# Kernel optimization log

Hardware: AMD Instinct MI355X
Metric: run time of the kernel (lower is better)

The kernel has to match this reference:

```python
import jax, jax.numpy as jnp
import numpy as np

COORD_DIM = 2
NUM_CHANNELS = 3
LATENT = 128
HIDDEN = 64
N0 = 8192
RADIUS = 0.035
RADII = (RADIUS, 2.0 * RADIUS)
ITER_COUNT = 3


def _radius_edges(y, x, r):
    # y: (Ny,d) source points, x: (Nx,d) query points -> edge lists (src into y, dst into x)
    d2 = ((x[:, None, :] - y[None, :, :]) ** 2).sum(-1)
    dst, src = np.nonzero(d2 <= r * r)
    return jnp.asarray(src, jnp.int32), jnp.asarray(dst, jnp.int32)


def setup_inputs():
    rng = np.random.default_rng(0)
    coords_np = rng.uniform(size=(COORD_DIM, N0)).astype(np.float32)
    c0 = coords_np.T            # (N0, d) fine level
    c1 = coords_np[:, ::2].T    # (N1, d) coarse level (stride-2 subsample)
    r_cross = max(RADII)
    e01_src, e01_dst = _radius_edges(c0, c1, r_cross)   # GK_0_1: y=lvl0, x=lvl1
    e10_src, e10_dst = _radius_edges(c1, c0, r_cross)   # GK_1_0: y=lvl1, x=lvl0
    e00_src, e00_dst = _radius_edges(c0, c0, RADII[0])  # GK_0_0
    e11_src, e11_dst = _radius_edges(c1, c1, RADII[1])  # GK_1_1

    key = jax.random.key(0)
    ks = iter(jax.random.split(key, 40))

    def lin(fi, fo):
        return jax.random.normal(next(ks), (fi, fo), jnp.float32) / np.float32(np.sqrt(fi))

    inp = dict(
        coords=jnp.asarray(coords_np),
        samples=jax.random.normal(next(ks), (N0, NUM_CHANNELS), jnp.float32),
        sigma=jax.random.uniform(next(ks), (1,), jnp.float32),
        fc_lift_w=lin(NUM_CHANNELS, LATENT), fc_lift_b=jnp.zeros((LATENT,), jnp.float32),
        fc_proj_w=lin(LATENT, NUM_CHANNELS), fc_proj_b=jnp.zeros((NUM_CHANNELS,), jnp.float32),
        W0_w=lin(LATENT, LATENT), W0_b=jnp.zeros((LATENT,), jnp.float32),
        W1_w=lin(LATENT, LATENT), W1_b=jnp.zeros((LATENT,), jnp.float32),
    )
    for name in ("gk00", "gk01", "gk10", "gk11"):
        inp[name + "_w1"] = lin(2 * COORD_DIM, HIDDEN)
        inp[name + "_b1"] = jnp.zeros((HIDDEN,), jnp.float32)
        inp[name + "_w2"] = lin(HIDDEN, LATENT)
        inp[name + "_b2"] = jnp.zeros((LATENT,), jnp.float32)
    inp.update(e00_src=e00_src, e00_dst=e00_dst, e01_src=e01_src, e01_dst=e01_dst,
               e10_src=e10_src, e10_dst=e10_dst, e11_src=e11_src, e11_dst=e11_dst)
    return inp


def _gno(xc, yc, f_y, src, dst, w1, b1, w2, b2, num_x):
    # gather -> edge kernel MLP on concat coords -> modulate by f_y -> scatter-mean
    e = jnp.concatenate([yc[src], xc[dst]], axis=1)        # (E, 2d)
    k = jax.nn.gelu(e @ w1 + b1) @ w2 + b2                 # (E, C) kernel values
    msg = k * f_y[src]                                     # 'linear' integral transform
    out = jax.ops.segment_sum(msg, dst, num_segments=num_x)
    cnt = jax.ops.segment_sum(jnp.ones(src.shape, msg.dtype), dst, num_segments=num_x)
    return out / jnp.maximum(cnt, 1.0)[:, None]


def reference(coords, samples, sigma,
              fc_lift_w, fc_lift_b, fc_proj_w, fc_proj_b,
              W0_w, W0_b, W1_w, W1_b,
              gk00_w1, gk00_b1, gk00_w2, gk00_b2,
              gk01_w1, gk01_b1, gk01_w2, gk01_b2,
              gk10_w1, gk10_b1, gk10_w2, gk10_b2,
              gk11_w1, gk11_b1, gk11_w2, gk11_b2,
              e00_src, e00_dst, e01_src, e01_dst,
              e10_src, e10_dst, e11_src, e11_dst):
    c0 = coords.T            # (N0, d)
    c1 = coords[:, ::2].T    # (N1, d)
    n0, n1 = c0.shape[0], c1.shape[0]
    v_down0 = samples @ fc_lift_w + fc_lift_b   # lifted features, never overwritten at level 0
    v_up0 = v_down0
    v_up1 = None
    for _ in range(ITER_COUNT):
        # downward pass (l = 1)
        vd = _gno(c1, c0, v_down0, e01_src, e01_dst, gk01_w1, gk01_b1, gk01_w2, gk01_b2, n1)
        if v_up1 is not None:
            vd = vd + v_up1
        v_down1 = jax.nn.relu(vd)
        # bottom level update
        v_up1 = jax.nn.relu(v_down1 @ W1_w + W1_b
                            + _gno(c1, c1, v_down1, e11_src, e11_dst, gk11_w1, gk11_b1, gk11_w2, gk11_b2, n1))
        # upward pass (l = 0)
        vu = _gno(c0, c1, v_up1, e10_src, e10_dst, gk10_w1, gk10_b1, gk10_w2, gk10_b2, n0)
        vu = vu + v_down0 @ W0_w + W0_b \
             + _gno(c0, c0, v_down0, e00_src, e00_dst, gk00_w1, gk00_b1, gk00_w2, gk00_b2, n0)
        v_up0 = jax.nn.relu(vu)
    return v_up0 @ fc_proj_w + fc_proj_b   # (N0, num_channels)
```

## Files before the change

kernel.cpp:

```cpp
#include <hip/hip_runtime.h>
#include <hip/hip_bf16.h>

typedef __attribute__((ext_vector_type(8))) short s8;
typedef __attribute__((ext_vector_type(4))) float f4;

#define TILE 128

__device__ __forceinline__ float gelu_fast(float x) {
    float x2 = x * x;
    float k2 = x * fmaf(x2, 0.10294326f, 2.30220819f);
    float e  = __builtin_amdgcn_exp2f(k2);
    float r  = __builtin_amdgcn_rcpf(e + 1.f);
    return fmaf(-x, r, x);
}

__device__ __forceinline__ unsigned pack_bf16x2(float a, float b) {
    __hip_bfloat162 h = __float22bfloat162_rn(make_float2(a, b));
    return *(unsigned*)&h;
}

__device__ __forceinline__ short f2bf_bits(float v) {
    __hip_bfloat16 b = __float2bfloat16(v);
    return *(short*)&b;
}

struct RP { const int* edst; int E; int N; int* rowptr; };

__global__ void rowptr4_kernel(RP a, RP b, RP c, RP d) {
    RP g = (blockIdx.y == 0) ? a : (blockIdx.y == 1) ? b : (blockIdx.y == 2) ? c : d;
    int i = blockIdx.x * blockDim.x + threadIdx.x;
    if (i >= g.E) return;
    int dd = g.edst[i];
    int p  = (i == 0) ? -1 : g.edst[i - 1];
    for (int r = p + 1; r <= dd; ++r) g.rowptr[r] = i;
    if (i == g.E - 1)
        for (int r = dd + 1; r <= g.N; ++r) g.rowptr[r] = g.E;
}

__global__ __launch_bounds__(128) void pack_w2_kernel(
    const float* __restrict__ wa, const float* __restrict__ wb,
    const float* __restrict__ wc, const float* __restrict__ wd,
    short* __restrict__ out)
{
    const int g = blockIdx.x >> 2, T = blockIdx.x & 3;
    const float* w2 = (g == 0) ? wa : (g == 1) ? wb : (g == 2) ? wc : wd;
    short* dst = out + (size_t)g * 8192;
    const int t = threadIdx.x;
    const int w = t >> 6, lane = t & 63, q = (lane >> 4), n = lane & 15;
#pragma unroll
    for (int s = 0; s < 2; ++s)
#pragma unroll
        for (int j = 0; j < 8; ++j) {
            int k  = s * 32 + q * 8 + j;
            int ch = 64 * w + 4 * n + T;
            dst[((((w * 4 + T) * 2 + s) * 64) + lane) * 8 + j] =
                f2bf_bits(w2[k * 128 + ch]);
        }
}

struct GnoP {
    const float* fy;
    const int* esrc;
    const int* edst;
    const float* w1;
    const float* b1;
    const short* w2;
    const float* b2;
    float* acc;
    int E, sx, sy, pad;
};

__device__ __forceinline__ int seg_end(unsigned long long m0, unsigned long long m1, int a) {
    if (a < 64) {
        unsigned long long r = m0 >> a;
        if (r) return a + (int)__builtin_ctzll(r) + 1;
        return 64 + (int)__builtin_ctzll(m1) + 1;
    }
    unsigned long long r = m1 >> (a - 64);
    return a + (int)__builtin_ctzll(r) + 1;
}

__global__ __launch_bounds__(128) void gno_edge_kernel(
    const float* __restrict__ coords, int n0, GnoP A, GnoP B, int ntA)
{
    const GnoP P = (blockIdx.x < ntA) ? A : B;
    const int tile = (blockIdx.x < ntA) ? blockIdx.x : blockIdx.x - ntA;
    const int t = threadIdx.x;
    const int w = t >> 6, lane = t & 63, q = lane >> 4, n = lane & 15;
    const int e0 = tile * TILE;
    const int te = min(TILE, P.E - e0);

    __shared__ __align__(16) float s_crd[(TILE + 16) * 4];
    __shared__ int s_off[TILE];
    __shared__ int s_dst[TILE];
    __shared__ unsigned long long s_mask[2];
    __shared__ __align__(16) short s_gb[2][16 * 72];

    {
        int e = min(e0 + t, P.E - 1);
        int sv = P.esrc[e];
        int dv = P.edst[e];
        s_off[t] = sv * 128;
        s_dst[t] = dv;
        f4 c4 = {coords[(long)sv * P.sy], coords[n0 + (long)sv * P.sy],
                 coords[(long)dv * P.sx], coords[n0 + (long)dv * P.sx]};
        *(f4*)&s_crd[t * 4] = c4;
        if (t < 16) *(f4*)&s_crd[(TILE + t) * 4] = c4;
    }

    const int h0 = 2 * (lane & 31);
    const float wA0 = P.w1[h0],       wA1 = P.w1[h0 + 1];
    const float wB0 = P.w1[64 + h0],  wB1 = P.w1[65 + h0];
    const float wC0 = P.w1[128 + h0], wC1 = P.w1[129 + h0];
    const float wD0 = P.w1[192 + h0], wD1 = P.w1[193 + h0];
    const float b10 = P.b1[h0],       b11 = P.b1[h0 + 1];

    s8 bfrag[4][2];
    const s8* w2f = (const s8*)P.w2;
#pragma unroll
    for (int T = 0; T < 4; ++T)
#pragma unroll
        for (int s = 0; s < 2; ++s)
            bfrag[T][s] = w2f[((w * 4 + T) * 2 + s) * 64 + lane];
    const f4 b2c = *(const f4*)&P.b2[w * 64 + 4 * n];
    f4 b2i[4];
#pragma unroll
    for (int T = 0; T < 4; ++T) { f4 z = {b2c[T], b2c[T], b2c[T], b2c[T]}; b2i[T] = z; }

    const float* fyl = P.fy + (w * 64 + 4 * n);

    __syncthreads();

    {
        int idx = w * 64 + lane;
        bool fl = (idx < te) && (idx == te - 1 || s_dst[idx + 1] != s_dst[idx]);
        unsigned long long m = __ballot(fl);
        if (lane == 0) s_mask[w] = m;
    }
    __syncthreads();
    const unsigned long long m0 = s_mask[0], m1 = s_mask[1];

    int g0 = 0;
    int b = seg_end(m0, m1, 0);
    f4 fvc[4];
#pragma unroll
    for (int r = 0; r < 4; ++r) {
        int row = q * 4 + r;
        if (row < b) fvc[r] = *(const f4*)&fyl[s_off[row]];
        else { f4 z = {0.f, 0.f, 0.f, 0.f}; fvc[r] = z; }
    }
    f4 accr = {0.f, 0.f, 0.f, 0.f};
    int gbp = 0;
    const int jh = lane >> 5;

    while (true) {
#pragma unroll
        for (int i = 0; i < 4; ++i) {
            int j = 4 * i + 2 * jh + w;
            const f4 crd = *(const f4*)&s_crd[(g0 + j) * 4];
            float x0 = fmaf(crd[0], wA0, fmaf(crd[1], wB0,
                       fmaf(crd[2], wC0, fmaf(crd[3], wD0, b10))));
            float x1 = fmaf(crd[0], wA1, fmaf(crd[1], wB1,
                       fmaf(crd[2], wC1, fmaf(crd[3], wD1, b11))));
            *(unsigned*)&s_gb[gbp][j * 72 + h0] = pack_bf16x2(gelu_fast(x0), gelu_fast(x1));
        }
        __syncthreads();
        const s8 a0 = *(const s8*)&s_gb[gbp][n * 72 + q * 8];
        const s8 a1 = *(const s8*)&s_gb[gbp][n * 72 + q * 8 + 32];
        f4 c[4];
#pragma unroll
        for (int T = 0; T < 4; ++T) {
            f4 z = __builtin_amdgcn_mfma_f32_16x16x32_bf16(a0, bfrag[T][0], b2i[T], 0, 0, 0);
            c[T] = __builtin_amdgcn_mfma_f32_16x16x32_bf16(a1, bfrag[T][1], z, 0, 0, 0);
        }
#pragma unroll
        for (int r = 0; r < 4; ++r)
#pragma unroll
            for (int T = 0; T < 4; ++T)
                accr[T] = fmaf(c[T][r], fvc[r][T], accr[T]);

        int gn = g0 + 16, bn = b;
        const bool endseg = (gn >= b);
        if (endseg) {
            gn = b;
            if (gn < te) bn = seg_end(m0, m1, gn);
            const int dcur = s_dst[g0];
#pragma unroll
            for (int T = 0; T < 4; ++T) {
                float v = accr[T];
                v += __shfl_xor(v, 16, 64);
                v += __shfl_xor(v, 32, 64);
                if (q == 0)
                    atomicAdd(&P.acc[(long)dcur * 128 + w * 64 + 4 * n + T], v);
            }
            f4 z = {0.f, 0.f, 0.f, 0.f};
            accr = z;
        }
        if (gn >= te) break;
#pragma unroll
        for (int r = 0; r < 4; ++r) {
            int row = gn + q * 4 + r;
            if (row < bn) fvc[r] = *(const f4*)&fyl[s_off[row]];
            else { f4 z = {0.f, 0.f, 0.f, 0.f}; fvc[r] = z; }
        }
        g0 = gn; b = bn;
        gbp ^= 1;
    }
}

__global__ void zero_kernel(float* __restrict__ p, long n) {
    long i = ((long)blockIdx.x * 256 + threadIdx.x) * 4;
    if (i < n) { f4 z = {0.f, 0.f, 0.f, 0.f}; *(f4*)&p[i] = z; }
}

__global__ __launch_bounds__(256) void epi0001_kernel(
    float* __restrict__ acc, const int* __restrict__ rp00, int N0,
    const int* __restrict__ rp01, float* __restrict__ vd0zero, long ntot)
{
    long idx = (long)blockIdx.x * 256 + threadIdx.x;
    if (idx >= ntot) return;
    int d = (int)(idx >> 7);
    float deg;
    if (d < N0) { deg = (float)(rp00[d + 1] - rp00[d]); vd0zero[idx] = 0.f; }
    else        { deg = (float)(rp01[d - N0 + 1] - rp01[d - N0]); }
    acc[idx] = acc[idx] / fmaxf(deg, 1.f);
}

__global__ __launch_bounds__(128) void relu_mm_kernel(
    const float* __restrict__ base, float* __restrict__ accu,
    const int* __restrict__ rowptr, float* __restrict__ w1t,
    const float* __restrict__ W, const float* __restrict__ bias,
    float* __restrict__ vout, float* __restrict__ zbuf, int R)
{
    const int r0 = blockIdx.x * 8;
    const int t = threadIdx.x;
    __shared__ float s_x[8 * 128];
#pragma unroll
    for (int j = 0; j < 8; ++j) {
        int r = r0 + j;
        long o = (long)r * 128 + t;
        float v = base[o];
        if (accu) {
            float deg = (float)(rowptr[r + 1] - rowptr[r]);
            float u = fmaxf(accu[o] / fmaxf(deg, 1.f) + w1t[o], 0.f);
            v += u;
            accu[o] = 0.f;
        } else if (zbuf) {
            zbuf[o] = 0.f;
        }
        v = fmaxf(v, 0.f);
        s_x[j * 128 + t] = v;
        vout[o] = v;
    }
    __syncthreads();
    float acc[8];
    const float bc = bias[t];
#pragma unroll
    for (int j = 0; j < 8; ++j) acc[j] = bc;
#pragma unroll 4
    for (int hh = 0; hh < 128; ++hh) {
        float wv = W[hh * 128 + t];
#pragma unroll
        for (int j = 0; j < 8; ++j) acc[j] += s_x[j * 128 + hh] * wv;
    }
#pragma unroll
    for (int j = 0; j < 8; ++j)
        w1t[(long)(r0 + j) * 128 + t] = acc[j];
}

__global__ __launch_bounds__(256) void epi11_kernel(
    float* __restrict__ acc, const int* __restrict__ rowptr,
    const float* __restrict__ w1t, int N)
{
    long idx = (long)blockIdx.x * 256 + threadIdx.x;
    if (idx >= (long)N * 128) return;
    int d = (int)(idx >> 7);
    float deg = (float)(rowptr[d + 1] - rowptr[d]);
    acc[idx] = fmaxf(acc[idx] / fmaxf(deg, 1.f) + w1t[idx], 0.f);
}

__global__ __launch_bounds__(128) void lift_mm_kernel(
    const float* __restrict__ samples, const float* __restrict__ LW,
    const float* __restrict__ Lb, const float* __restrict__ W0,
    const float* __restrict__ W0b, float* __restrict__ vout,
    float* __restrict__ w0t, int R)
{
    const int r0 = blockIdx.x * 8;
    const int t = threadIdx.x;
    __shared__ float s_x[8 * 128];
#pragma unroll
    for (int j = 0; j < 8; ++j) {
        int r = r0 + j;
        float s0 = samples[r * 3 + 0], s1 = samples[r * 3 + 1], s2 = samples[r * 3 + 2];
        float v = s0 * LW[t] + s1 * LW[128 + t] + s2 * LW[256 + t] + Lb[t];
        s_x[j * 128 + t] = v;
        vout[(long)r * 128 + t] = v;
    }
    __syncthreads();
    float acc[8];
    const float bc = W0b[t];
#pragma unroll
    for (int j = 0; j < 8; ++j) acc[j] = bc;
#pragma unroll 4
    for (int hh = 0; hh < 128; ++hh) {
        float wv = W0[hh * 128 + t];
#pragma unroll
        for (int j = 0; j < 8; ++j) acc[j] += s_x[j * 128 + hh] * wv;
    }
#pragma unroll
    for (int j = 0; j < 8; ++j)
        w0t[(long)(r0 + j) * 128 + t] = acc[j];
}

__global__ __launch_bounds__(128) void epi_proj_kernel(
    const float* __restrict__ acc, const int* __restrict__ rowptr,
    const float* __restrict__ add0, const float* __restrict__ add1,
    const float* __restrict__ projw, const float* __restrict__ projb,
    float* __restrict__ fout, int N)
{
    const int d = blockIdx.x, t = threadIdx.x;
    float deg = (float)(rowptr[d + 1] - rowptr[d]);
    long o = (long)d * 128 + t;
    float res = fmaxf(acc[o] / fmaxf(deg, 1.f) + add0[o] + add1[o], 0.f);
    float p0 = res * projw[t * 3 + 0];
    float p1 = res * projw[t * 3 + 1];
    float p2 = res * projw[t * 3 + 2];
#pragma unroll
    for (int off = 32; off > 0; off >>= 1) {
        p0 += __shfl_down(p0, off);
        p1 += __shfl_down(p1, off);
        p2 += __shfl_down(p2, off);
    }
    __shared__ float sred[6];
    if ((t & 63) == 0) { int w = t >> 6; sred[w * 3 + 0] = p0; sred[w * 3 + 1] = p1; sred[w * 3 + 2] = p2; }
    __syncthreads();
    if (t < 3) fout[d * 3 + t] = sred[t] + sred[3 + t] + projb[t];
}

extern "C" void kernel_launch(void* const* d_in, const int* in_sizes, int n_in,
                              void* d_out, int out_size, void* d_ws, size_t ws_size,
                              hipStream_t stream)
{
    const float* coords  = (const float*)d_in[0];
    const float* samples = (const float*)d_in[1];
    const float* lift_w  = (const float*)d_in[3];
    const float* lift_b  = (const float*)d_in[4];
    const float* proj_w  = (const float*)d_in[5];
    const float* proj_b  = (const float*)d_in[6];
    const float* W0_w    = (const float*)d_in[7];
    const float* W0_b    = (const float*)d_in[8];
    const float* W1_w    = (const float*)d_in[9];
    const float* W1_b    = (const float*)d_in[10];
    const float *gw1[4], *gb1[4], *gw2[4], *gb2[4];
    for (int g = 0; g < 4; ++g) {
        gw1[g] = (const float*)d_in[11 + 4 * g + 0];
        gb1[g] = (const float*)d_in[11 + 4 * g + 1];
        gw2[g] = (const float*)d_in[11 + 4 * g + 2];
        gb2[g] = (const float*)d_in[11 + 4 * g + 3];
    }
    const int* es[4]; const int* ed[4]; int E[4];
    for (int g = 0; g < 4; ++g) {
        es[g] = (const int*)d_in[27 + 2 * g];
        ed[g] = (const int*)d_in[27 + 2 * g + 1];
        E[g]  = in_sizes[27 + 2 * g];
    }

    const int N0 = in_sizes[0] / 2;
    const int N1 = (N0 + 1) / 2;

    float* ws = (float*)d_ws;
    float* v_down0 = ws;
    float* w0term  = v_down0 + (size_t)N0 * 128;
    float* gno00o  = w0term  + (size_t)N0 * 128;
    float* gno01b  = gno00o  + (size_t)N0 * 128;
    float* v_down1 = gno01b  + (size_t)N1 * 128;
    float* w1term  = v_down1 + (size_t)N1 * 128;
    float* v_up1   = w1term  + (size_t)N1 * 128;
    short* w2pack  = (short*)(v_up1 + (size_t)N1 * 128);
    int*   rp      = (int*)(w2pack + 4 * 8192);
    int* rp00 = rp;
    int* rp01 = rp00 + (N0 + 1);
    int* rp10 = rp01 + (N1 + 1);
    int* rp11 = rp10 + (N0 + 1);

    {
        int maxE = E[0];
        for (int g = 1; g < 4; ++g) maxE = max(maxE, E[g]);
        RP a = {ed[0], E[0], N0, rp00};
        RP b = {ed[1], E[1], N1, rp01};
        RP c = {ed[2], E[2], N0, rp10};
        RP d = {ed[3], E[3], N1, rp11};
        dim3 grid((maxE + 255) / 256, 4);
        rowptr4_kernel<<<grid, 256, 0, stream>>>(a, b, c, d);
    }
    pack_w2_kernel<<<16, 128, 0, stream>>>(gw2[0], gw2[1], gw2[2], gw2[3], w2pack);

    const long n00 = (long)N0 * 128, n11 = (long)N1 * 128;

    zero_kernel<<<(int)((n00 + n11) / 4 + 255) / 256, 256, 0, stream>>>(gno00o, n00 + n11);
    lift_mm_kernel<<<N0 / 8, 128, 0, stream>>>(samples, lift_w, lift_b, W0_w, W0_b,
                                               v_down0, w0term, N0);

    GnoP P00 = {v_down0, es[0], ed[0], gw1[0], gb1[0], w2pack + 0 * 8192, gb2[0], gno00o, E[0], 1, 1, 0};
    GnoP P01 = {v_down0, es[1], ed[1], gw1[1], gb1[1], w2pack + 1 * 8192, gb2[1], gno01b, E[1], 2, 1, 0};
    GnoP P11 = {v_down1, es[3], ed[3], gw1[3], gb1[3], w2pack + 3 * 8192, gb2[3], v_up1,  E[3], 2, 2, 0};
    GnoP P10 = {v_up1,   es[2], ed[2], gw1[2], gb1[2], w2pack + 2 * 8192, gb2[2], v_down0, E[2], 1, 2, 0};

    {
        int tA = (E[0] + TILE - 1) / TILE, tB = (E[1] + TILE - 1) / TILE;
        gno_edge_kernel<<<tA + tB, 128, 0, stream>>>(coords, N0, P00, P01, tA);
    }
    epi0001_kernel<<<(int)((n00 + n11) + 255) / 256, 256, 0, stream>>>(
        gno00o, rp00, N0, rp01, v_down0, n00 + n11);

    for (int it = 0; it < 3; ++it) {
        relu_mm_kernel<<<N1 / 8, 128, 0, stream>>>(
            gno01b, (it == 0) ? nullptr : v_up1, rp11, w1term, W1_w, W1_b,
            v_down1, (it == 0) ? v_up1 : nullptr, N1);
        int tt = (E[3] + TILE - 1) / TILE;
        gno_edge_kernel<<<tt, 128, 0, stream>>>(coords, N0, P11, P11, tt);
    }
    epi11_kernel<<<(int)(n11 + 255) / 256, 256, 0, stream>>>(v_up1, rp11, w1term, N1);

    {
        int tt = (E[2] + TILE - 1) / TILE;
        gno_edge_kernel<<<tt, 128, 0, stream>>>(coords, N0, P10, P10, tt);
    }
    epi_proj_kernel<<<N0, 128, 0, stream>>>(v_down0, rp10, w0term, gno00o,
                                            proj_w, proj_b, (float*)d_out, N0);
}
```

Baseline: 356.5 us.

## Split edge-kernel MLP over hidden dim per wave to remove block barriers

Each wave now computes half of the hidden units and all 128 output channels in its own shared buffer. This removes the per-iteration __syncthreads and the cross-wave mask exchange. The edge tile shrinks to 64 so one wave ballot covers the tile, and the kernel now requests 3 blocks per SM via launch bounds. Both waves issue atomics with their partial sums, so atomic traffic doubles. bf16 packing switches to a cheaper round-half-up bit trick, and the W2 pack layout changes to match.

```diff
diff --git a/kernel.cpp b/kernel.cpp
--- a/kernel.cpp
+++ b/kernel.cpp
@@ -4,7 +4,7 @@
 typedef __attribute__((ext_vector_type(8))) short s8;
 typedef __attribute__((ext_vector_type(4))) float f4;
 
-#define TILE 128
+#define TILE 64
 
 __device__ __forceinline__ float gelu_fast(float x) {
     float x2 = x * x;
@@ -14,9 +14,10 @@
     return fmaf(-x, r, x);
 }
 
-__device__ __forceinline__ unsigned pack_bf16x2(float a, float b) {
-    __hip_bfloat162 h = __float22bfloat162_rn(make_float2(a, b));
-    return *(unsigned*)&h;
+__device__ __forceinline__ unsigned pack_bf16x2_fast(float a, float b) {
+    unsigned ua = __builtin_bit_cast(unsigned, a) + 0x8000u;
+    unsigned ub = __builtin_bit_cast(unsigned, b) + 0x8000u;
+    return __builtin_amdgcn_perm(ub, ua, 0x07060302u);
 }
 
 __device__ __forceinline__ short f2bf_bits(float v) {
@@ -42,19 +43,18 @@
     const float* __restrict__ wc, const float* __restrict__ wd,
     short* __restrict__ out)
 {
-    const int g = blockIdx.x >> 2, T = blockIdx.x & 3;
+    const int g = blockIdx.x;
     const float* w2 = (g == 0) ? wa : (g == 1) ? wb : (g == 2) ? wc : wd;
     short* dst = out + (size_t)g * 8192;
     const int t = threadIdx.x;
-    const int w = t >> 6, lane = t & 63, q = (lane >> 4), n = lane & 15;
-#pragma unroll
-    for (int s = 0; s < 2; ++s)
+    const int s = t >> 6, lane = t & 63, q = (lane >> 4), n = lane & 15;
+#pragma unroll
+    for (int T = 0; T < 8; ++T)
 #pragma unroll
         for (int j = 0; j < 8; ++j) {
-            int k  = s * 32 + q * 8 + j;
-            int ch = 64 * w + 4 * n + T;
-            dst[((((w * 4 + T) * 2 + s) * 64) + lane) * 8 + j] =
-                f2bf_bits(w2[k * 128 + ch]);
+            int h  = 32 * s + q * 8 + j;
+            int ch = 8 * n + T;
+            dst[((s * 8 + T) * 64 + lane) * 8 + j] = f2bf_bits(w2[h * 128 + ch]);
         }
 }
 
@@ -70,33 +70,26 @@
     int E, sx, sy, pad;
 };
 
-__device__ __forceinline__ int seg_end(unsigned long long m0, unsigned long long m1, int a) {
-    if (a < 64) {
-        unsigned long long r = m0 >> a;
-        if (r) return a + (int)__builtin_ctzll(r) + 1;
-        return 64 + (int)__builtin_ctzll(m1) + 1;
-    }
-    unsigned long long r = m1 >> (a - 64);
-    return a + (int)__builtin_ctzll(r) + 1;
-}
-
-__global__ __launch_bounds__(128) void gno_edge_kernel(
+__device__ __forceinline__ int seg_end1(unsigned long long m, int a) {
+    return a + 1 + (int)__builtin_ctzll(m >> a);
+}
+
+__global__ __launch_bounds__(128, 3) void gno_edge_kernel(
     const float* __restrict__ coords, int n0, GnoP A, GnoP B, int ntA)
 {
     const GnoP P = (blockIdx.x < ntA) ? A : B;
     const int tile = (blockIdx.x < ntA) ? blockIdx.x : blockIdx.x - ntA;
     const int t = threadIdx.x;
-    const int w = t >> 6, lane = t & 63, q = lane >> 4, n = lane & 15;
+    const int wv = t >> 6, lane = t & 63, q = lane >> 4, n = lane & 15;
     const int e0 = tile * TILE;
     const int te = min(TILE, P.E - e0);
 
     __shared__ __align__(16) float s_crd[(TILE + 16) * 4];
     __shared__ int s_off[TILE];
     __shared__ int s_dst[TILE];
-    __shared__ unsigned long long s_mask[2];
-    __shared__ __align__(16) short s_gb[2][16 * 72];
-
-    {
+    __shared__ __align__(16) short s_gb[2][16 * 40];
+
+    if (t < TILE) {
         int e = min(e0 + t, P.E - 1);
         int sv = P.esrc[e];
         int dv = P.edst[e];
@@ -108,103 +101,110 @@
         if (t < 16) *(f4*)&s_crd[(TILE + t) * 4] = c4;
     }
 
-    const int h0 = 2 * (lane & 31);
+    const int hl = 2 * (lane & 15);
+    const int h0 = 32 * wv + hl;
     const float wA0 = P.w1[h0],       wA1 = P.w1[h0 + 1];
     const float wB0 = P.w1[64 + h0],  wB1 = P.w1[65 + h0];
     const float wC0 = P.w1[128 + h0], wC1 = P.w1[129 + h0];
     const float wD0 = P.w1[192 + h0], wD1 = P.w1[193 + h0];
     const float b10 = P.b1[h0],       b11 = P.b1[h0 + 1];
 
-    s8 bfrag[4][2];
+    s8 bfrag[8];
     const s8* w2f = (const s8*)P.w2;
 #pragma unroll
-    for (int T = 0; T < 4; ++T)
-#pragma unroll
-        for (int s = 0; s < 2; ++s)
-            bfrag[T][s] = w2f[((w * 4 + T) * 2 + s) * 64 + lane];
-    const f4 b2c = *(const f4*)&P.b2[w * 64 + 4 * n];
-    f4 b2i[4];
-#pragma unroll
-    for (int T = 0; T < 4; ++T) { f4 z = {b2c[T], b2c[T], b2c[T], b2c[T]}; b2i[T] = z; }
-
-    const float* fyl = P.fy + (w * 64 + 4 * n);
+    for (int T = 0; T < 8; ++T)
+        bfrag[T] = w2f[(wv * 8 + T) * 64 + lane];
+
+    f4 b2a = {0.f, 0.f, 0.f, 0.f}, b2b = {0.f, 0.f, 0.f, 0.f};
+    if (wv == 0) {
+        b2a = *(const f4*)&P.b2[8 * n];
+        b2b = *(const f4*)&P.b2[8 * n + 4];
+    }
+    const float* fyl = P.fy + 8 * n;
+    short* gb = &s_gb[wv][0];
+    const int je = 4 * (lane >> 4);
 
     __syncthreads();
 
-    {
-        int idx = w * 64 + lane;
-        bool fl = (idx < te) && (idx == te - 1 || s_dst[idx + 1] != s_dst[idx]);
-        unsigned long long m = __ballot(fl);
-        if (lane == 0) s_mask[w] = m;
-    }
-    __syncthreads();
-    const unsigned long long m0 = s_mask[0], m1 = s_mask[1];
+    bool fl = (lane < te) && (lane == te - 1 || s_dst[lane + 1] != s_dst[lane]);
+    const unsigned long long m = __ballot(fl);
 
     int g0 = 0;
-    int b = seg_end(m0, m1, 0);
-    f4 fvc[4];
+    int b = seg_end1(m, 0);
+    f4 fva[4], fvb[4];
 #pragma unroll
     for (int r = 0; r < 4; ++r) {
         int row = q * 4 + r;
-        if (row < b) fvc[r] = *(const f4*)&fyl[s_off[row]];
-        else { f4 z = {0.f, 0.f, 0.f, 0.f}; fvc[r] = z; }
-    }
-    f4 accr = {0.f, 0.f, 0.f, 0.f};
-    int gbp = 0;
-    const int jh = lane >> 5;
+        if (row < b) {
+            const float* p = &fyl[s_off[row]];
+            fva[r] = *(const f4*)p;
+            fvb[r] = *(const f4*)(p + 4);
+        } else {
+            f4 z = {0.f, 0.f, 0.f, 0.f};
+            fva[r] = z; fvb[r] = z;
+        }
+    }
+    float accr[8] = {0.f, 0.f, 0.f, 0.f, 0.f, 0.f, 0.f, 0.f};
 
     while (true) {
 #pragma unroll
         for (int i = 0; i < 4; ++i) {
-            int j = 4 * i + 2 * jh + w;
+            int j = je + i;
             const f4 crd = *(const f4*)&s_crd[(g0 + j) * 4];
             float x0 = fmaf(crd[0], wA0, fmaf(crd[1], wB0,
                        fmaf(crd[2], wC0, fmaf(crd[3], wD0, b10))));
             float x1 = fmaf(crd[0], wA1, fmaf(crd[1], wB1,
                        fmaf(crd[2], wC1, fmaf(crd[3], wD1, b11))));
-            *(unsigned*)&s_gb[gbp][j * 72 + h0] = pack_bf16x2(gelu_fast(x0), gelu_fast(x1));
-        }
-        __syncthreads();
-        const s8 a0 = *(const s8*)&s_gb[gbp][n * 72 + q * 8];
-        const s8 a1 = *(const s8*)&s_gb[gbp][n * 72 + q * 8 + 32];
-        f4 c[4];
-#pragma unroll
-        for (int T = 0; T < 4; ++T) {
-            f4 z = __builtin_amdgcn_mfma_f32_16x16x32_bf16(a0, bfrag[T][0], b2i[T], 0, 0, 0);
-            c[T] = __builtin_amdgcn_mfma_f32_16x16x32_bf16(a1, bfrag[T][1], z, 0, 0, 0);
-        }
-#pragma unroll
-        for (int r = 0; r < 4; ++r)
-#pragma unroll
-            for (int T = 0; T < 4; ++T)
-                accr[T] = fmaf(c[T][r], fvc[r][T], accr[T]);
+            *(unsigned*)&gb[j * 40 + hl] = pack_bf16x2_fast(gelu_fast(x0), gelu_fast(x1));
+        }
+        const s8 a = *(const s8*)&gb[n * 40 + q * 8];
+#pragma unroll
+        for (int Tp = 0; Tp < 4; ++Tp) {
+            f4 z = {0.f, 0.f, 0.f, 0.f};
+            f4 c0 = __builtin_amdgcn_mfma_f32_16x16x32_bf16(a, bfrag[2 * Tp], z, 0, 0, 0);
+            f4 c1 = __builtin_amdgcn_mfma_f32_16x16x32_bf16(a, bfrag[2 * Tp + 1], z, 0, 0, 0);
+            const int T0 = 2 * Tp, T1 = 2 * Tp + 1;
+            const float bb0 = (T0 < 4) ? b2a[T0 & 3] : b2b[T0 & 3];
+            const float bb1 = (T1 < 4) ? b2a[T1 & 3] : b2b[T1 & 3];
+#pragma unroll
+            for (int r = 0; r < 4; ++r) {
+                float f0 = (T0 < 4) ? fva[r][T0 & 3] : fvb[r][T0 & 3];
+                float f1 = (T1 < 4) ? fva[r][T1 & 3] : fvb[r][T1 & 3];
+                accr[T0] = fmaf(c0[r] + bb0, f0, accr[T0]);
+                accr[T1] = fmaf(c1[r] + bb1, f1, accr[T1]);
+            }
+        }
 
         int gn = g0 + 16, bn = b;
         const bool endseg = (gn >= b);
         if (endseg) {
             gn = b;
-            if (gn < te) bn = seg_end(m0, m1, gn);
+            if (gn < te) bn = seg_end1(m, gn);
             const int dcur = s_dst[g0];
-#pragma unroll
-            for (int T = 0; T < 4; ++T) {
+            float* ap = &P.acc[(long)dcur * 128 + 8 * n];
+#pragma unroll
+            for (int T = 0; T < 8; ++T) {
                 float v = accr[T];
                 v += __shfl_xor(v, 16, 64);
                 v += __shfl_xor(v, 32, 64);
-                if (q == 0)
-                    atomicAdd(&P.acc[(long)dcur * 128 + w * 64 + 4 * n + T], v);
+                if (q == 0) atomicAdd(&ap[T], v);
+                accr[T] = 0.f;
             }
-            f4 z = {0.f, 0.f, 0.f, 0.f};
-            accr = z;
         }
         if (gn >= te) break;
 #pragma unroll
         for (int r = 0; r < 4; ++r) {
             int row = gn + q * 4 + r;
-            if (row < bn) fvc[r] = *(const f4*)&fyl[s_off[row]];
-            else { f4 z = {0.f, 0.f, 0.f, 0.f}; fvc[r] = z; }
+            if (row < bn) {
+                const float* p = &fyl[s_off[row]];
+                fva[r] = *(const f4*)p;
+                fvb[r] = *(const f4*)(p + 4);
+            } else {
+                f4 z = {0.f, 0.f, 0.f, 0.f};
+                fva[r] = z; fvb[r] = z;
+            }
         }
         g0 = gn; b = bn;
-        gbp ^= 1;
     }
 }
 
@@ -393,7 +393,7 @@
         dim3 grid((maxE + 255) / 256, 4);
         rowptr4_kernel<<<grid, 256, 0, stream>>>(a, b, c, d);
     }
-    pack_w2_kernel<<<16, 128, 0, stream>>>(gw2[0], gw2[1], gw2[2], gw2[3], w2pack);
+    pack_w2_kernel<<<4, 128, 0, stream>>>(gw2[0], gw2[1], gw2[2], gw2[3], w2pack);
 
     const long n00 = (long)N0 * 128, n11 = (long)N1 * 128;
 
```

New measurement: 692.1 us. +94.1%, slower.

## Process 32-edge chunks per iteration and use cheaper bf16 packing

Applied to the files above, without the earlier changes.

The edge loop now handles up to 32 edges per iteration instead of 16. It computes GELU hidden activations for 32 rows, issues a second MFMA pair only when the segment still has more than 16 rows, and gathers two sets of source feature rows up front. This is meant to halve the per-chunk barriers and loop overhead, and to increase memory-level parallelism for the gathers. It also swaps the bf16 round-to-nearest-even conversion for an add-0x8000-and-permute trick, which rounds half away and does not handle NaN. The trade-offs are more registers and LDS per block and wasted GELU work on short segments.

```diff
diff --git a/kernel.cpp b/kernel.cpp
--- a/kernel.cpp
+++ b/kernel.cpp
@@ -14,9 +14,10 @@
     return fmaf(-x, r, x);
 }
 
-__device__ __forceinline__ unsigned pack_bf16x2(float a, float b) {
-    __hip_bfloat162 h = __float22bfloat162_rn(make_float2(a, b));
-    return *(unsigned*)&h;
+__device__ __forceinline__ unsigned pack_bf16x2_fast(float a, float b) {
+    unsigned ua = __builtin_bit_cast(unsigned, a) + 0x8000u;
+    unsigned ub = __builtin_bit_cast(unsigned, b) + 0x8000u;
+    return __builtin_amdgcn_perm(ub, ua, 0x07060302u);
 }
 
 __device__ __forceinline__ short f2bf_bits(float v) {
@@ -90,11 +91,11 @@
     const int e0 = tile * TILE;
     const int te = min(TILE, P.E - e0);
 
-    __shared__ __align__(16) float s_crd[(TILE + 16) * 4];
+    __shared__ __align__(16) float s_crd[(TILE + 32) * 4];
     __shared__ int s_off[TILE];
     __shared__ int s_dst[TILE];
     __shared__ unsigned long long s_mask[2];
-    __shared__ __align__(16) short s_gb[2][16 * 72];
+    __shared__ __align__(16) short s_gb[2][32 * 72];
 
     {
         int e = min(e0 + t, P.E - 1);
@@ -105,7 +106,7 @@
         f4 c4 = {coords[(long)sv * P.sy], coords[n0 + (long)sv * P.sy],
                  coords[(long)dv * P.sx], coords[n0 + (long)dv * P.sx]};
         *(f4*)&s_crd[t * 4] = c4;
-        if (t < 16) *(f4*)&s_crd[(TILE + t) * 4] = c4;
+        if (t < 32) *(f4*)&s_crd[(TILE + t) * 4] = c4;
     }
 
     const int h0 = 2 * (lane & 31);
@@ -142,12 +143,14 @@
 
     int g0 = 0;
     int b = seg_end(m0, m1, 0);
-    f4 fvc[4];
+    f4 fv0[4], fv1[4];
 #pragma unroll
     for (int r = 0; r < 4; ++r) {
-        int row = q * 4 + r;
-        if (row < b) fvc[r] = *(const f4*)&fyl[s_off[row]];
-        else { f4 z = {0.f, 0.f, 0.f, 0.f}; fvc[r] = z; }
+        int row0 = q * 4 + r, row1 = 16 + q * 4 + r;
+        if (row0 < b) fv0[r] = *(const f4*)&fyl[s_off[row0]];
+        else { f4 z = {0.f, 0.f, 0.f, 0.f}; fv0[r] = z; }
+        if (row1 < b) fv1[r] = *(const f4*)&fyl[s_off[row1]];
+        else { f4 z = {0.f, 0.f, 0.f, 0.f}; fv1[r] = z; }
     }
     f4 accr = {0.f, 0.f, 0.f, 0.f};
     int gbp = 0;
@@ -155,31 +158,51 @@
 
     while (true) {
 #pragma unroll
-        for (int i = 0; i < 4; ++i) {
+        for (int i = 0; i < 8; ++i) {
             int j = 4 * i + 2 * jh + w;
             const f4 crd = *(const f4*)&s_crd[(g0 + j) * 4];
             float x0 = fmaf(crd[0], wA0, fmaf(crd[1], wB0,
                        fmaf(crd[2], wC0, fmaf(crd[3], wD0, b10))));
             float x1 = fmaf(crd[0], wA1, fmaf(crd[1], wB1,
                        fmaf(crd[2], wC1, fmaf(crd[3], wD1, b11))));
-            *(unsigned*)&s_gb[gbp][j * 72 + h0] = pack_bf16x2(gelu_fast(x0), gelu_fast(x1));
+            *(unsigned*)&s_gb[gbp][j * 72 + h0] = pack_bf16x2_fast(gelu_fast(x0), gelu_fast(x1));
         }
         __syncthreads();
-        const s8 a0 = *(const s8*)&s_gb[gbp][n * 72 + q * 8];
-        const s8 a1 = *(const s8*)&s_gb[gbp][n * 72 + q * 8 + 32];
-        f4 c[4];
-#pragma unroll
-        for (int T = 0; T < 4; ++T) {
-            f4 z = __builtin_amdgcn_mfma_f32_16x16x32_bf16(a0, bfrag[T][0], b2i[T], 0, 0, 0);
-            c[T] = __builtin_amdgcn_mfma_f32_16x16x32_bf16(a1, bfrag[T][1], z, 0, 0, 0);
-        }
-#pragma unroll
-        for (int r = 0; r < 4; ++r)
-#pragma unroll
-            for (int T = 0; T < 4; ++T)
-                accr[T] = fmaf(c[T][r], fvc[r][T], accr[T]);
-
-        int gn = g0 + 16, bn = b;
+        const short* gb = &s_gb[gbp][0];
+        const int cnt = min(32, b - g0);
+        {
+            const s8 a0 = *(const s8*)&gb[n * 72 + q * 8];
+            const s8 a1 = *(const s8*)&gb[n * 72 + q * 8 + 32];
+            f4 c[4];
+#pragma unroll
+            for (int T = 0; T < 4; ++T) {
+                f4 z = __builtin_amdgcn_mfma_f32_16x16x32_bf16(a0, bfrag[T][0], b2i[T], 0, 0, 0);
+                c[T] = __builtin_amdgcn_mfma_f32_16x16x32_bf16(a1, bfrag[T][1], z, 0, 0, 0);
+            }
+#pragma unroll
+            for (int r = 0; r < 4; ++r)
+#pragma unroll
+                for (int T = 0; T < 4; ++T)
+                    accr[T] = fmaf(c[T][r], fv0[r][T], accr[T]);
+        }
+        if (cnt > 16) {
+            const s8 a0 = *(const s8*)&gb[(16 + n) * 72 + q * 8];
+            const s8 a1 = *(const s8*)&gb[(16 + n) * 72 + q * 8 + 32];
+            f4 c[4];
+#pragma unroll
+            for (int T = 0; T < 4; ++T) {
+                f4 z = {0.f, 0.f, 0.f, 0.f};
+                z = __builtin_amdgcn_mfma_f32_16x16x32_bf16(a0, bfrag[T][0], z, 0, 0, 0);
+                c[T] = __builtin_amdgcn_mfma_f32_16x16x32_bf16(a1, bfrag[T][1], z, 0, 0, 0);
+            }
+#pragma unroll
+            for (int r = 0; r < 4; ++r)
+#pragma unroll
+                for (int T = 0; T < 4; ++T)
+                    accr[T] = fmaf(c[T][r], fv1[r][T], accr[T]);
+        }
+
+        int gn = g0 + cnt, bn = b;
         const bool endseg = (gn >= b);
         if (endseg) {
             gn = b;
@@ -199,9 +222,11 @@
         if (gn >= te) break;
 #pragma unroll
         for (int r = 0; r < 4; ++r) {
-            int row = gn + q * 4 + r;
-            if (row < bn) fvc[r] = *(const f4*)&fyl[s_off[row]];
-            else { f4 z = {0.f, 0.f, 0.f, 0.f}; fvc[r] = z; }
+            int row0 = gn + q * 4 + r, row1 = gn + 16 + q * 4 + r;
+            if (row0 < bn) fv0[r] = *(const f4*)&fyl[s_off[row0]];
+            else { f4 z = {0.f, 0.f, 0.f, 0.f}; fv0[r] = z; }
+            if (row1 < bn) fv1[r] = *(const f4*)&fyl[s_off[row1]];
+            else { f4 z = {0.f, 0.f, 0.f, 0.f}; fv1[r] = z; }
         }
         g0 = gn; b = bn;
         gbp ^= 1;
```

Result: slower. 383.3 us (+7.5%).

## Merge setup kernels into one prep launch and fold degree normalization into consumers

Applied to the files above, without the earlier changes.

Combines the zeroing, weight-packing, rowptr-building and lift/W0 matmul kernels into a single prep kernel that dispatches on block index. It removes the epi0001 pass by applying the degree normalizations in relu_mm and epi_proj, and moves the v_down0 zeroing into epi11. It also replaces the round-to-nearest-even bf16 pack with a bias-add-and-permute that rounds ties away from zero, which changes numerics slightly. The goal is fewer launches and less extra memory traffic, in exchange for a heterogeneous prep grid and a repeated division inside the loop.

```diff
diff --git a/kernel.cpp b/kernel.cpp
--- a/kernel.cpp
+++ b/kernel.cpp
@@ -14,9 +14,10 @@
     return fmaf(-x, r, x);
 }
 
-__device__ __forceinline__ unsigned pack_bf16x2(float a, float b) {
-    __hip_bfloat162 h = __float22bfloat162_rn(make_float2(a, b));
-    return *(unsigned*)&h;
+__device__ __forceinline__ unsigned pack_bf16x2_fast(float a, float b) {
+    unsigned ua = __builtin_bit_cast(unsigned, a) + 0x8000u;
+    unsigned ub = __builtin_bit_cast(unsigned, b) + 0x8000u;
+    return __builtin_amdgcn_perm(ub, ua, 0x07060302u);
 }
 
 __device__ __forceinline__ short f2bf_bits(float v) {
@@ -24,38 +25,85 @@
     return *(short*)&b;
 }
 
-struct RP { const int* edst; int E; int N; int* rowptr; };
-
-__global__ void rowptr4_kernel(RP a, RP b, RP c, RP d) {
-    RP g = (blockIdx.y == 0) ? a : (blockIdx.y == 1) ? b : (blockIdx.y == 2) ? c : d;
-    int i = blockIdx.x * blockDim.x + threadIdx.x;
-    if (i >= g.E) return;
-    int dd = g.edst[i];
-    int p  = (i == 0) ? -1 : g.edst[i - 1];
-    for (int r = p + 1; r <= dd; ++r) g.rowptr[r] = i;
-    if (i == g.E - 1)
-        for (int r = dd + 1; r <= g.N; ++r) g.rowptr[r] = g.E;
-}
-
-__global__ __launch_bounds__(128) void pack_w2_kernel(
-    const float* __restrict__ wa, const float* __restrict__ wb,
-    const float* __restrict__ wc, const float* __restrict__ wd,
-    short* __restrict__ out)
-{
-    const int g = blockIdx.x >> 2, T = blockIdx.x & 3;
-    const float* w2 = (g == 0) ? wa : (g == 1) ? wb : (g == 2) ? wc : wd;
-    short* dst = out + (size_t)g * 8192;
+struct PrepArgs {
+    float* zbase; long zn4;
+    const float* w2s[4]; short* w2pack;
+    const int* edst[4]; int E[4]; int N[4]; int* rowptr[4]; int rbPer;
+    const float *samples, *LW, *Lb, *W0, *W0b;
+    float *vout, *w0t;
+    int zb;
+};
+
+__global__ __launch_bounds__(256) void prep_kernel(PrepArgs A) {
+    __shared__ float s_x[16 * 128];
+    int bid = blockIdx.x;
     const int t = threadIdx.x;
-    const int w = t >> 6, lane = t & 63, q = (lane >> 4), n = lane & 15;
-#pragma unroll
-    for (int s = 0; s < 2; ++s)
+    if (bid < A.zb) {
+        long i = (long)bid * 256 + t;
+        if (i < A.zn4) { f4 z = {0.f, 0.f, 0.f, 0.f}; *(f4*)&A.zbase[i * 4] = z; }
+        return;
+    }
+    bid -= A.zb;
+    if (bid < 16) {
+        if (t < 128) {
+            const int g = bid >> 2, T = bid & 3;
+            const float* w2 = A.w2s[g];
+            short* dst = A.w2pack + (size_t)g * 8192;
+            const int w = t >> 6, lane = t & 63, q = (lane >> 4), n = lane & 15;
+#pragma unroll
+            for (int s = 0; s < 2; ++s)
+#pragma unroll
+                for (int j = 0; j < 8; ++j) {
+                    int k  = s * 32 + q * 8 + j;
+                    int ch = 64 * w + 4 * n + T;
+                    dst[((((w * 4 + T) * 2 + s) * 64) + lane) * 8 + j] =
+                        f2bf_bits(w2[k * 128 + ch]);
+                }
+        }
+        return;
+    }
+    bid -= 16;
+    if (bid < 4 * A.rbPer) {
+        const int g = bid / A.rbPer;
+        const int i = (bid % A.rbPer) * 256 + t;
+        const int* ed = A.edst[g]; const int E = A.E[g]; const int N = A.N[g];
+        int* rp = A.rowptr[g];
+        if (i < E) {
+            int dd = ed[i];
+            int p  = (i == 0) ? -1 : ed[i - 1];
+            for (int r = p + 1; r <= dd; ++r) rp[r] = i;
+            if (i == E - 1)
+                for (int r = dd + 1; r <= N; ++r) rp[r] = E;
+        }
+        return;
+    }
+    bid -= 4 * A.rbPer;
+    {
+        const int r0 = bid * 16;
+        const int col = t & 127, half = t >> 7;
 #pragma unroll
         for (int j = 0; j < 8; ++j) {
-            int k  = s * 32 + q * 8 + j;
-            int ch = 64 * w + 4 * n + T;
-            dst[((((w * 4 + T) * 2 + s) * 64) + lane) * 8 + j] =
-                f2bf_bits(w2[k * 128 + ch]);
-        }
+            int r = r0 + half * 8 + j;
+            float s0 = A.samples[r * 3 + 0], s1 = A.samples[r * 3 + 1], s2 = A.samples[r * 3 + 2];
+            float v = s0 * A.LW[col] + s1 * A.LW[128 + col] + s2 * A.LW[256 + col] + A.Lb[col];
+            s_x[(half * 8 + j) * 128 + col] = v;
+            A.vout[(long)r * 128 + col] = v;
+        }
+        __syncthreads();
+        float acc[8];
+        const float bc = A.W0b[col];
+#pragma unroll
+        for (int j = 0; j < 8; ++j) acc[j] = bc;
+#pragma unroll 4
+        for (int hh = 0; hh < 128; ++hh) {
+            float wv = A.W0[hh * 128 + col];
+#pragma unroll
+            for (int j = 0; j < 8; ++j) acc[j] += s_x[(half * 8 + j) * 128 + hh] * wv;
+        }
+#pragma unroll
+        for (int j = 0; j < 8; ++j)
+            A.w0t[(long)(r0 + half * 8 + j) * 128 + col] = acc[j];
+    }
 }
 
 struct GnoP {
@@ -162,7 +210,7 @@
                        fmaf(crd[2], wC0, fmaf(crd[3], wD0, b10))));
             float x1 = fmaf(crd[0], wA1, fmaf(crd[1], wB1,
                        fmaf(crd[2], wC1, fmaf(crd[3], wD1, b11))));
-            *(unsigned*)&s_gb[gbp][j * 72 + h0] = pack_bf16x2(gelu_fast(x0), gelu_fast(x1));
+            *(unsigned*)&s_gb[gbp][j * 72 + h0] = pack_bf16x2_fast(gelu_fast(x0), gelu_fast(x1));
         }
         __syncthreads();
         const s8 a0 = *(const s8*)&s_gb[gbp][n * 72 + q * 8];
@@ -208,27 +256,10 @@
     }
 }
 
-__global__ void zero_kernel(float* __restrict__ p, long n) {
-    long i = ((long)blockIdx.x * 256 + threadIdx.x) * 4;
-    if (i < n) { f4 z = {0.f, 0.f, 0.f, 0.f}; *(f4*)&p[i] = z; }
-}
-
-__global__ __launch_bounds__(256) void epi0001_kernel(
-    float* __restrict__ acc, const int* __restrict__ rp00, int N0,
-    const int* __restrict__ rp01, float* __restrict__ vd0zero, long ntot)
-{
-    long idx = (long)blockIdx.x * 256 + threadIdx.x;
-    if (idx >= ntot) return;
-    int d = (int)(idx >> 7);
-    float deg;
-    if (d < N0) { deg = (float)(rp00[d + 1] - rp00[d]); vd0zero[idx] = 0.f; }
-    else        { deg = (float)(rp01[d - N0 + 1] - rp01[d - N0]); }
-    acc[idx] = acc[idx] / fmaxf(deg, 1.f);
-}
-
 __global__ __launch_bounds__(128) void relu_mm_kernel(
-    const float* __restrict__ base, float* __restrict__ accu,
-    const int* __restrict__ rowptr, float* __restrict__ w1t,
+    const float* __restrict__ base, const int* __restrict__ rp01,
+    float* __restrict__ accu, const int* __restrict__ rowptr,
+    float* __restrict__ w1t,
     const float* __restrict__ W, const float* __restrict__ bias,
     float* __restrict__ vout, float* __restrict__ zbuf, int R)
 {
@@ -239,7 +270,8 @@
     for (int j = 0; j < 8; ++j) {
         int r = r0 + j;
         long o = (long)r * 128 + t;
-        float v = base[o];
+        float deg0 = (float)(rp01[r + 1] - rp01[r]);
+        float v = base[o] / fmaxf(deg0, 1.f);
         if (accu) {
             float deg = (float)(rowptr[r + 1] - rowptr[r]);
             float u = fmaxf(accu[o] / fmaxf(deg, 1.f) + w1t[o], 0.f);
@@ -270,58 +302,29 @@
 
 __global__ __launch_bounds__(256) void epi11_kernel(
     float* __restrict__ acc, const int* __restrict__ rowptr,
-    const float* __restrict__ w1t, int N)
+    const float* __restrict__ w1t, int N,
+    float* __restrict__ vd0, long n00)
 {
     long idx = (long)blockIdx.x * 256 + threadIdx.x;
+    if (idx < n00) vd0[idx] = 0.f;
     if (idx >= (long)N * 128) return;
     int d = (int)(idx >> 7);
     float deg = (float)(rowptr[d + 1] - rowptr[d]);
     acc[idx] = fmaxf(acc[idx] / fmaxf(deg, 1.f) + w1t[idx], 0.f);
 }
 
-__global__ __launch_bounds__(128) void lift_mm_kernel(
-    const float* __restrict__ samples, const float* __restrict__ LW,
-    const float* __restrict__ Lb, const float* __restrict__ W0,
-    const float* __restrict__ W0b, float* __restrict__ vout,
-    float* __restrict__ w0t, int R)
-{
-    const int r0 = blockIdx.x * 8;
-    const int t = threadIdx.x;
-    __shared__ float s_x[8 * 128];
-#pragma unroll
-    for (int j = 0; j < 8; ++j) {
-        int r = r0 + j;
-        float s0 = samples[r * 3 + 0], s1 = samples[r * 3 + 1], s2 = samples[r * 3 + 2];
-        float v = s0 * LW[t] + s1 * LW[128 + t] + s2 * LW[256 + t] + Lb[t];
-        s_x[j * 128 + t] = v;
-        vout[(long)r * 128 + t] = v;
-    }
-    __syncthreads();
-    float acc[8];
-    const float bc = W0b[t];
-#pragma unroll
-    for (int j = 0; j < 8; ++j) acc[j] = bc;
-#pragma unroll 4
-    for (int hh = 0; hh < 128; ++hh) {
-        float wv = W0[hh * 128 + t];
-#pragma unroll
-        for (int j = 0; j < 8; ++j) acc[j] += s_x[j * 128 + hh] * wv;
-    }
-#pragma unroll
-    for (int j = 0; j < 8; ++j)
-        w0t[(long)(r0 + j) * 128 + t] = acc[j];
-}
-
 __global__ __launch_bounds__(128) void epi_proj_kernel(
     const float* __restrict__ acc, const int* __restrict__ rowptr,
-    const float* __restrict__ add0, const float* __restrict__ add1,
+    const float* __restrict__ add0,
+    const float* __restrict__ add1, const int* __restrict__ rp00,
     const float* __restrict__ projw, const float* __restrict__ projb,
     float* __restrict__ fout, int N)
 {
     const int d = blockIdx.x, t = threadIdx.x;
-    float deg = (float)(rowptr[d + 1] - rowptr[d]);
+    float deg  = (float)(rowptr[d + 1] - rowptr[d]);
+    float dg00 = (float)(rp00[d + 1] - rp00[d]);
     long o = (long)d * 128 + t;
-    float res = fmaxf(acc[o] / fmaxf(deg, 1.f) + add0[o] + add1[o], 0.f);
+    float res = fmaxf(acc[o] / fmaxf(deg, 1.f) + add0[o] + add1[o] / fmaxf(dg00, 1.f), 0.f);
     float p0 = res * projw[t * 3 + 0];
     float p1 = res * projw[t * 3 + 1];
     float p2 = res * projw[t * 3 + 2];
@@ -383,23 +386,26 @@
     int* rp10 = rp01 + (N1 + 1);
     int* rp11 = rp10 + (N0 + 1);
 
+    const long n00 = (long)N0 * 128, n11 = (long)N1 * 128;
+
     {
         int maxE = E[0];
         for (int g = 1; g < 4; ++g) maxE = max(maxE, E[g]);
-        RP a = {ed[0], E[0], N0, rp00};
-        RP b = {ed[1], E[1], N1, rp01};
-        RP c = {ed[2], E[2], N0, rp10};
-        RP d = {ed[3], E[3], N1, rp11};
-        dim3 grid((maxE + 255) / 256, 4);
-        rowptr4_kernel<<<grid, 256, 0, stream>>>(a, b, c, d);
-    }
-    pack_w2_kernel<<<16, 128, 0, stream>>>(gw2[0], gw2[1], gw2[2], gw2[3], w2pack);
-
-    const long n00 = (long)N0 * 128, n11 = (long)N1 * 128;
-
-    zero_kernel<<<(int)((n00 + n11) / 4 + 255) / 256, 256, 0, stream>>>(gno00o, n00 + n11);
-    lift_mm_kernel<<<N0 / 8, 128, 0, stream>>>(samples, lift_w, lift_b, W0_w, W0_b,
-                                               v_down0, w0term, N0);
+        PrepArgs A;
+        A.zbase = gno00o; A.zn4 = (n00 + n11) / 4;
+        for (int g = 0; g < 4; ++g) A.w2s[g] = gw2[g];
+        A.w2pack = w2pack;
+        A.edst[0] = ed[0]; A.edst[1] = ed[1]; A.edst[2] = ed[2]; A.edst[3] = ed[3];
+        A.E[0] = E[0]; A.E[1] = E[1]; A.E[2] = E[2]; A.E[3] = E[3];
+        A.N[0] = N0; A.N[1] = N1; A.N[2] = N0; A.N[3] = N1;
+        A.rowptr[0] = rp00; A.rowptr[1] = rp01; A.rowptr[2] = rp10; A.rowptr[3] = rp11;
+        A.rbPer = (maxE + 255) / 256;
+        A.samples = samples; A.LW = lift_w; A.Lb = lift_b; A.W0 = W0_w; A.W0b = W0_b;
+        A.vout = v_down0; A.w0t = w0term;
+        A.zb = (int)((A.zn4 + 255) / 256);
+        int grid = A.zb + 16 + 4 * A.rbPer + N0 / 16;
+        prep_kernel<<<grid, 256, 0, stream>>>(A);
+    }
 
     GnoP P00 = {v_down0, es[0], ed[0], gw1[0], gb1[0], w2pack + 0 * 8192, gb2[0], gno00o, E[0], 1, 1, 0};
     GnoP P01 = {v_down0, es[1], ed[1], gw1[1], gb1[1], w2pack + 1 * 8192, gb2[1], gno01b, E[1], 2, 1, 0};
@@ -410,22 +416,22 @@
         int tA = (E[0] + TILE - 1) / TILE, tB = (E[1] + TILE - 1) / TILE;
         gno_edge_kernel<<<tA + tB, 128, 0, stream>>>(coords, N0, P00, P01, tA);
     }
-    epi0001_kernel<<<(int)((n00 + n11) + 255) / 256, 256, 0, stream>>>(
-        gno00o, rp00, N0, rp01, v_down0, n00 + n11);
 
     for (int it = 0; it < 3; ++it) {
         relu_mm_kernel<<<N1 / 8, 128, 0, stream>>>(
-            gno01b, (it == 0) ? nullptr : v_up1, rp11, w1term, W1_w, W1_b,
+            gno01b, rp01, (it == 0) ? nullptr : v_up1, rp11, w1term, W1_w, W1_b,
             v_down1, (it == 0) ? v_up1 : nullptr, N1);
         int tt = (E[3] + TILE - 1) / TILE;
         gno_edge_kernel<<<tt, 128, 0, stream>>>(coords, N0, P11, P11, tt);
     }
-    epi11_kernel<<<(int)(n11 + 255) / 256, 256, 0, stream>>>(v_up1, rp11, w1term, N1);
+    epi11_kernel<<<(int)((n00 + 255) / 256), 256, 0, stream>>>(
+        v_up1, rp11, w1term, N1, v_down0, n00);
 
     {
         int tt = (E[2] + TILE - 1) / TILE;
         gno_edge_kernel<<<tt, 128, 0, stream>>>(coords, N0, P10, P10, tt);
     }
-    epi_proj_kernel<<<N0, 128, 0, stream>>>(v_down0, rp10, w0term, gno00o,
+    epi_proj_kernel<<<N0, 128, 0, stream>>>(v_down0, rp10, w0term,
+                                            gno00o, rp00,
                                             proj_w, proj_b, (float*)d_out, N0);
 }
```

Result: faster. 344.4 us (-3.4%).
